# Kernel optimization log

Measured on AMD Instinct MI355X. Metric: run time of the kernel, lower is better.

The kernel has to match this reference:

```python
import jax, jax.numpy as jnp
import numpy as np

N, LQ, D_MODEL, M_HEADS, P_POINTS, H_DIM, W_DIM = 8, 4096, 256, 8, 4, 64, 64


def setup_inputs() -> dict:
    key = jax.random.key(0)
    ks = jax.random.split(key, 9)
    d = D_MODEL
    scale = 1.0 / np.sqrt(d).astype(np.float32)
    return {
        "query": jax.random.normal(ks[0], (N, LQ, d), jnp.float32),
        "reference_points": jax.random.uniform(ks[1], (N, LQ, 2), jnp.float32),
        "input_flatten": jax.random.normal(ks[2], (N, H_DIM * W_DIM, d), jnp.float32),
        "H": H_DIM,
        "W": W_DIM,
        "Wv": jax.random.normal(ks[3], (d, d), jnp.float32) * scale,
        "bv": jnp.zeros((d,), jnp.float32),
        "Woff": jax.random.normal(ks[4], (M_HEADS * P_POINTS * 2, d), jnp.float32) * 0.01,
        "boff": jax.random.normal(ks[5], (M_HEADS * P_POINTS * 2,), jnp.float32) * 0.5,
        "Wa": jax.random.normal(ks[6], (M_HEADS * P_POINTS, d), jnp.float32) * 0.01,
        "ba": jnp.zeros((M_HEADS * P_POINTS,), jnp.float32),
        "Wo": jax.random.normal(ks[7], (d, d), jnp.float32) * scale,
        "bo": jnp.zeros((d,), jnp.float32),
    }


def _bilinear_sample(val, grid, H, W):
    # val: [B, D, H*W]; grid: [B, Lq, P, 2] in [-1, 1] (x, y); align_corners=False, zero padding.
    B, D, _ = val.shape
    _, Lq, P, _ = grid.shape
    x = (grid[..., 0] + 1.0) * (W * 0.5) - 0.5
    y = (grid[..., 1] + 1.0) * (H * 0.5) - 0.5
    x0 = jnp.floor(x)
    y0 = jnp.floor(y)
    x0i = x0.astype(jnp.int32)
    y0i = y0.astype(jnp.int32)
    wx1 = x - x0
    wy1 = y - y0
    out = jnp.zeros((B, D, Lq, P), val.dtype)
    for xi, wx in ((x0i, 1.0 - wx1), (x0i + 1, wx1)):
        for yi, wy in ((y0i, 1.0 - wy1), (y0i + 1, wy1)):
            valid = (xi >= 0) & (xi < W) & (yi >= 0) & (yi < H)
            idx = jnp.clip(yi, 0, H - 1) * W + jnp.clip(xi, 0, W - 1)  # [B, Lq, P]
            g = jnp.take_along_axis(val, idx.reshape(B, 1, Lq * P), axis=2).reshape(B, D, Lq, P)
            w = jnp.where(valid, wx * wy, 0.0)
            out = out + g * w[:, None]
    return out


def reference(query, reference_points, input_flatten, H, W, Wv, bv, Woff, boff, Wa, ba, Wo, bo):
    n, lq, d = query.shape
    m, p = M_HEADS, P_POINTS
    dh = d // m
    value = (input_flatten @ Wv.T + bv).reshape(n, H * W, m, dh)
    offsets = (query @ Woff.T + boff).reshape(n, lq, m, p, 2)
    attw = jax.nn.softmax((query @ Wa.T + ba).reshape(n, lq, m, p), axis=-1)
    normalizer = jnp.array([W, H], dtype=query.dtype)  # [W, H] order per torch code
    loc = reference_points[:, :, None, None, :] + offsets / normalizer
    grid = 2.0 * loc - 1.0  # [n, lq, m, p, 2]
    # value -> [n*m, dh, H*W] matching torch flatten(2).transpose(1,2).reshape
    val = jnp.transpose(value, (0, 2, 3, 1)).reshape(n * m, dh, H * W)
    grd = jnp.transpose(grid, (0, 2, 1, 3, 4)).reshape(n * m, lq, p, 2)
    samp = _bilinear_sample(val, grd, H, W)  # [n*m, dh, lq, p]
    aw = jnp.transpose(attw, (0, 2, 1, 3)).reshape(n * m, 1, lq, p)
    out = (samp * aw).sum(-1).reshape(n, m * dh, lq)
    out = jnp.transpose(out, (0, 2, 1))  # [n, lq, d]
    return out @ Wo.T + bo
```

## Files before the change

kernel.cpp:

```cpp
#include <hip/hip_runtime.h>
#include <math.h>

#define NB   8
#define LQN  4096
#define DM   256
#define MH   8
#define PP   4
#define HH   64
#define WW   64
#define LG   128
#define PW   67
#define PPIX (PW*PW)

typedef __bf16 bf16x8 __attribute__((ext_vector_type(8)));
typedef float  f32x4  __attribute__((ext_vector_type(4)));
typedef unsigned short us8 __attribute__((ext_vector_type(8)));
typedef unsigned short us4 __attribute__((ext_vector_type(4)));

__device__ __forceinline__ unsigned short f2bf(float f) {
    unsigned u = __float_as_uint(f);
    u += 0x7FFFu + ((u >> 16) & 1u);
    return (unsigned short)(u >> 16);
}
__device__ __forceinline__ float bf2f(unsigned short b) {
    return __uint_as_float((unsigned)b << 16);
}

__device__ __forceinline__ void gl2lds16(const void* g, unsigned short* l) {
    __builtin_amdgcn_global_load_lds(
        (const __attribute__((address_space(1))) void*)g,
        (__attribute__((address_space(3))) void*)l,
        16, 0, 0);
}

__device__ __forceinline__ bf16x8 cvt_frag(const unsigned short* s, int row, int kq) {
    const int u0 = row * 8 + ((kq * 2) ^ (row & 7));
    const int u1 = u0 ^ 1;
    const f32x4 a0 = *(const f32x4*)&s[u0 * 8];
    const f32x4 a1 = *(const f32x4*)&s[u1 * 8];
    bf16x8 v;
    v[0] = (__bf16)a0[0]; v[1] = (__bf16)a0[1];
    v[2] = (__bf16)a0[2]; v[3] = (__bf16)a0[3];
    v[4] = (__bf16)a1[0]; v[5] = (__bf16)a1[1];
    v[6] = (__bf16)a1[2]; v[7] = (__bf16)a1[3];
    return v;
}

__global__ __launch_bounds__(256)
void prep_kernel(const float* __restrict__ Wv, const float* __restrict__ Wo,
                 const float* __restrict__ Woff, const float* __restrict__ Wa,
                 const float* __restrict__ boff, const float* __restrict__ ba,
                 unsigned short* __restrict__ Wvh, unsigned short* __restrict__ Woh,
                 unsigned short* __restrict__ Wcath, float* __restrict__ bcat,
                 unsigned short* __restrict__ valueP) {
    const int i = blockIdx.x * 256 + threadIdx.x;
    if (i < 65536) {
        Wvh[i] = f2bf(Wv[i]);
    } else if (i < 131072) {
        const int j = i - 65536;
        Woh[j] = f2bf(Wo[j]);
    } else if (i < 163840) {
        const int j = i - 131072, n = j >> 8, k = j & 255;
        const float v = (n < 64) ? Woff[n * 256 + k]
                                 : ((n < 96) ? Wa[(n - 64) * 256 + k] : 0.f);
        Wcath[j] = f2bf(v);
    } else if (i < 163968) {
        const int n = i - 163840;
        bcat[n] = (n < 64) ? boff[n] : ((n < 96) ? ba[n - 64] : 0.f);
    } else if (i < 163968 + 201216) {
        const int j   = i - 163968;
        const int c4  = j & 63;
        const int pix = j >> 6;
        const int n   = pix / 393;
        const int r   = pix - n * 393;
        int x, y;
        if (r < 201) {
            const int q = r / 67;
            y = (q == 0) ? 0 : (q == 1 ? 65 : 66);
            x = r - q * 67;
        } else {
            const int q = r - 201;
            y = 1 + q / 3;
            const int s = q - (q / 3) * 3;
            x = (s == 0) ? 0 : (s == 1 ? 65 : 66);
        }
        const size_t addr = ((size_t)n * PPIX + (size_t)y * PW + x) * DM + c4 * 4;
        *(ushort4*)&valueP[addr] = make_ushort4(0, 0, 0, 0);
    }
}

__global__ __launch_bounds__(256, 4)
void dual_gemm(const float* __restrict__ Ain, const float* __restrict__ Aq,
               const unsigned short* __restrict__ Wvh,
               const unsigned short* __restrict__ Wcath,
               const float* __restrict__ bv, const float* __restrict__ bcat,
               unsigned short* __restrict__ valueP,
               unsigned short* __restrict__ logitsB) {
    constexpr int K = 256, NK = 8;
    __shared__ unsigned short sA[2][4096];
    __shared__ unsigned short sB[2][4096];

    const int t   = threadIdx.x;
    const int blk = blockIdx.x;
    const bool isVal = (blk < 1024);

    const float* A; const unsigned short* B; const float* bias;
    int brow, bcol;
    if (isVal) {
        const int x   = blk & 7;
        const int idx = blk >> 3;
        brow = x * 4096 + (idx >> 1) * 64;
        bcol = (idx & 1) * 128;
        A = Ain; B = Wvh; bias = bv;
    } else {
        const int blk2 = blk - 1024;
        brow = (blk2 & 7) * 4096 + (blk2 >> 3) * 64;
        bcol = 0;
        A = Aq; B = Wcath; bias = bcat;
    }

    const int srow = t >> 3;
    const int scq  = (t & 7) ^ (srow & 7);
    const float* aG = A + (size_t)(brow + srow) * K + scq * 4;
    const size_t aI = (size_t)32 * K;

    const unsigned short* bG = B + (size_t)(bcol + (t >> 2)) * K + (t & 3) * 8;
    const size_t bI = (size_t)64 * K;

    const int l   = t & 63;
    const int wid = t >> 6;
    const int wr  = wid >> 1, wc = wid & 1;
    const int fr  = l & 15,   kq = l >> 4;

    f32x4 acc[2][4] = {};

#define STAGE(buf, ks_) { const int k0_ = (ks_) * 32;                    \
       gl2lds16(aG + k0_,      &sA[buf][t * 8]);                         \
       gl2lds16(aG + k0_ + aI, &sA[buf][2048 + t * 8]);                  \
       gl2lds16(bG + k0_,      &sB[buf][t * 8]);                         \
       gl2lds16(bG + k0_ + bI, &sB[buf][2048 + t * 8]); }

    STAGE(0, 0);
    STAGE(1, 1);

    for (int ks = 0; ks < NK; ++ks) {
        const int cur = ks & 1;
        if (ks < NK - 1) asm volatile("s_waitcnt vmcnt(4)" ::: "memory");
        else             asm volatile("s_waitcnt vmcnt(0)" ::: "memory");
        __builtin_amdgcn_s_barrier();
        __builtin_amdgcn_sched_barrier(0);

        bf16x8 af[2], bf_[4];
#pragma unroll
        for (int m = 0; m < 2; ++m)
            af[m]  = cvt_frag(sA[cur], wr * 32 + m * 16 + fr, kq);
#pragma unroll
        for (int n = 0; n < 4; ++n)
            bf_[n] = *(const bf16x8*)&sB[cur][(wc * 64 + n * 16 + fr) * 32 + kq * 8];

#pragma unroll
        for (int m = 0; m < 2; ++m)
#pragma unroll
            for (int n = 0; n < 4; ++n)
                acc[m][n] = __builtin_amdgcn_mfma_f32_16x16x32_bf16(
                    bf_[n], af[m], acc[m][n], 0, 0, 0);

        __builtin_amdgcn_sched_barrier(0);
        __builtin_amdgcn_s_barrier();
        if (ks + 2 < NK) STAGE(cur, ks + 2);
    }
#undef STAGE

#pragma unroll
    for (int m = 0; m < 2; ++m) {
        const int row = brow + wr * 32 + m * 16 + fr;
        size_t rbase;
        if (isVal) {
            const int nb_ = row >> 12;
            const int pix = row & 4095;
            const int y   = pix >> 6, x = pix & 63;
            rbase = ((size_t)nb_ * PPIX + (size_t)(y + 1) * PW + (x + 1)) * DM;
        } else {
            rbase = (size_t)row * LG;
        }
#pragma unroll
        for (int n = 0; n < 4; ++n) {
            const int colq = bcol + wc * 64 + n * 16 + kq * 4;
            const float4 b4 = *(const float4*)&bias[colq];
            us4 o;
            o[0] = f2bf(acc[m][n][0] + b4.x);
            o[1] = f2bf(acc[m][n][1] + b4.y);
            o[2] = f2bf(acc[m][n][2] + b4.z);
            o[3] = f2bf(acc[m][n][3] + b4.w);
            *(us4*)&(isVal ? valueP : logitsB)[rbase + colq] = o;
        }
    }
}

__global__ __launch_bounds__(512, 4)
void fused_sample_out(const float* __restrict__ refp,
                      const unsigned short* __restrict__ valueP,
                      const unsigned short* __restrict__ logitsB,
                      const unsigned short* __restrict__ Woh,
                      const float* __restrict__ bo, float* __restrict__ C) {
    constexpr int K = 256, NK = 8;
    extern __shared__ unsigned short smem[];
    unsigned short* sS = smem;
    unsigned short* sB = smem + 16384;

    const int t    = threadIdx.x;
    const int blk  = blockIdx.x;
    const int nb   = blk & 7;
    const int brow = nb * 4096 + (blk >> 3) * 64;
    const int w    = t >> 6;
    const int lane = t & 63;

    {
        const int tp  = lane & 31;
        const int pm  = tp >> 2, ppt = tp & 3;
        const int half = lane >> 5;
        const int c8   = lane & 31;
        const int mh   = c8 >> 2;
        const unsigned short* vbase = valueP + (size_t)nb * (PPIX * DM) + c8 * 8;

        for (int i = 0; i < 8; ++i) {
            const int q = w * 8 + i;
            const int b = brow + q;
            const unsigned short* lg = logitsB + (size_t)b * LG;

            const float rx = refp[(size_t)b * 2 + 0];
            const float ry = refp[(size_t)b * 2 + 1];
            const float ox = bf2f(lg[pm * 8 + ppt * 2 + 0]);
            const float oy = bf2f(lg[pm * 8 + ppt * 2 + 1]);
            const float la = bf2f(lg[64 + tp]);

            const float x = fminf(fmaxf(fmaf(rx, (float)WW, ox) - 0.5f, -1.0f), 64.0f);
            const float y = fminf(fmaxf(fmaf(ry, (float)HH, oy) - 0.5f, -1.0f), 64.0f);

            float mx = fmaxf(la, __shfl_xor(la, 1));
            mx = fmaxf(mx, __shfl_xor(mx, 2));
            const float e = __expf(la - mx);
            float den = e + __shfl_xor(e, 1);
            den += __shfl_xor(den, 2);
            const float wgt = e / den;

            float accv[8] = {};
#pragma unroll
            for (int p = 0; p < PP; ++p) {
                const int   sl = mh * PP + p;
                const float xp = __shfl(x, sl);
                const float yp = __shfl(y, sl);
                const float wp = __shfl(wgt, sl);

                const float x0f = floorf(xp), y0f = floorf(yp);
                const int   x0 = (int)x0f,   y0 = (int)y0f;
                const float wx1 = xp - x0f,  wy1 = yp - y0f;
                const float wy  = half ? wy1 : (1.f - wy1);
                const float wA  = wp * wy * (1.f - wx1);
                const float wB  = wp * wy * wx1;

                const unsigned short* p0 =
                    vbase + (size_t)((y0 + 1 + half) * PW + (x0 + 1)) * DM;
                const us8 gA = *(const us8*)(p0);
                const us8 gB = *(const us8*)(p0 + DM);
#pragma unroll
                for (int j = 0; j < 8; ++j) {
                    accv[j] = fmaf(wA, bf2f(gA[j]), accv[j]);
                    accv[j] = fmaf(wB, bf2f(gB[j]), accv[j]);
                }
            }
#pragma unroll
            for (int j = 0; j < 8; ++j)
                accv[j] += __shfl_xor(accv[j], 32);

            if (half == 0) {
                us8 o;
#pragma unroll
                for (int j = 0; j < 8; ++j) o[j] = f2bf(accv[j]);
                *(us8*)&sS[q * 256 + ((c8 ^ (q & 7)) * 8)] = o;
            }
        }
    }
    __syncthreads();

    const unsigned short* bG = Woh + (size_t)(t >> 2) * K + (t & 3) * 8;
    const size_t rHalf = (size_t)128 * K;

    const int wr = w >> 2, wc = w & 3;
    const int fr = lane & 15, kq = lane >> 4;

    f32x4 acc[2][4] = {};

#define STAGEF(buf, ks_) { const int k0_ = (ks_) * 32;                   \
       gl2lds16(bG + k0_,         &sB[(buf) * 8192 + t * 8]);            \
       gl2lds16(bG + k0_ + rHalf, &sB[(buf) * 8192 + 4096 + t * 8]); }

    STAGEF(0, 0);
    STAGEF(1, 1);

    for (int ks = 0; ks < NK; ++ks) {
        const int cur = ks & 1;
        if (ks < NK - 1) asm volatile("s_waitcnt vmcnt(2)" ::: "memory");
        else             asm volatile("s_waitcnt vmcnt(0)" ::: "memory");
        __builtin_amdgcn_s_barrier();
        __builtin_amdgcn_sched_barrier(0);

        bf16x8 af[2], bfr[4];
#pragma unroll
        for (int m = 0; m < 2; ++m) {
            const int row = wr * 32 + m * 16 + fr;
            const int u   = (ks * 4 + kq) ^ (row & 7);
            af[m] = *(const bf16x8*)&sS[row * 256 + u * 8];
        }
#pragma unroll
        for (int n = 0; n < 4; ++n)
            bfr[n] = *(const bf16x8*)&sB[cur * 8192 + (wc * 64 + n * 16 + fr) * 32 + kq * 8];

#pragma unroll
        for (int m = 0; m < 2; ++m)
#pragma unroll
            for (int n = 0; n < 4; ++n)
                acc[m][n] = __builtin_amdgcn_mfma_f32_16x16x32_bf16(
                    bfr[n], af[m], acc[m][n], 0, 0, 0);

        __builtin_amdgcn_sched_barrier(0);
        __builtin_amdgcn_s_barrier();
        if (ks + 2 < NK) STAGEF(cur, ks + 2);
    }
#undef STAGEF

#pragma unroll
    for (int m = 0; m < 2; ++m) {
        const int row = brow + wr * 32 + m * 16 + fr;
#pragma unroll
        for (int n = 0; n < 4; ++n) {
            const int colq = wc * 64 + n * 16 + kq * 4;
            const float4 bs = *(const float4*)&bo[colq];
            float4 o;
            o.x = acc[m][n][0] + bs.x; o.y = acc[m][n][1] + bs.y;
            o.z = acc[m][n][2] + bs.z; o.w = acc[m][n][3] + bs.w;
            *(float4*)&C[(size_t)row * DM + colq] = o;
        }
    }
}

extern "C" void kernel_launch(void* const* d_in, const int* in_sizes, int n_in,
                              void* d_out, int out_size, void* d_ws, size_t ws_size,
                              hipStream_t stream) {
    const float* query  = (const float*)d_in[0];
    const float* refp   = (const float*)d_in[1];
    const float* inputf = (const float*)d_in[2];
    const float* Wv   = (const float*)d_in[5];
    const float* bv   = (const float*)d_in[6];
    const float* Woff = (const float*)d_in[7];
    const float* boff = (const float*)d_in[8];
    const float* Wa   = (const float*)d_in[9];
    const float* ba   = (const float*)d_in[10];
    const float* Wo   = (const float*)d_in[11];
    const float* bo   = (const float*)d_in[12];
    float* out = (float*)d_out;

    const int Mrows = NB * LQN;

    unsigned short* valueP   = (unsigned short*)d_ws;
    unsigned short* logitsB  = valueP   + (size_t)NB * PPIX * DM;
    unsigned short* Wvh      = logitsB  + (size_t)Mrows * LG;
    unsigned short* Woh      = Wvh      + 65536;
    unsigned short* Wcath    = Woh      + 65536;
    float*          bcat     = (float*)(Wcath + 32768);

    prep_kernel<<<1427, 256, 0, stream>>>(Wv, Wo, Woff, Wa, boff, ba,
                                          Wvh, Woh, Wcath, bcat, valueP);

    dual_gemm<<<1536, 256, 0, stream>>>(inputf, query, Wvh, Wcath, bv, bcat,
                                        valueP, logitsB);

    fused_sample_out<<<512, 512, 65536, stream>>>(refp, valueP, logitsB,
                                                  Woh, bo, out);
}
```

Measured before the change: 59.87 us.

## Fuse offset/attention-logit GEMM into the sampling-output kernel via LDS

Moves the query projection that produces sampling offsets and attention logits out of the combined GEMM launch and into the sampling/output kernel. Each block now computes its own 64x128 logits tile with MFMA and keeps it in LDS rather than writing it to a global buffer and reading it back. The aim is to remove that global round trip and let the value GEMM run alone with fewer blocks. In exchange, dynamic LDS grows to 80 KB per block, which may reduce occupancy. The query GEMM is also no longer overlapped with the value GEMM.

```diff
diff --git a/kernel.cpp b/kernel.cpp
--- a/kernel.cpp
+++ b/kernel.cpp
@@ -8,7 +8,6 @@
 #define PP   4
 #define HH   64
 #define WW   64
-#define LG   128
 #define PW   67
 #define PPIX (PW*PW)
 
@@ -90,41 +89,27 @@
 }
 
 __global__ __launch_bounds__(256, 4)
-void dual_gemm(const float* __restrict__ Ain, const float* __restrict__ Aq,
-               const unsigned short* __restrict__ Wvh,
-               const unsigned short* __restrict__ Wcath,
-               const float* __restrict__ bv, const float* __restrict__ bcat,
-               unsigned short* __restrict__ valueP,
-               unsigned short* __restrict__ logitsB) {
+void value_gemm(const float* __restrict__ Ain,
+                const unsigned short* __restrict__ Wvh,
+                const float* __restrict__ bv,
+                unsigned short* __restrict__ valueP) {
     constexpr int K = 256, NK = 8;
     __shared__ unsigned short sA[2][4096];
     __shared__ unsigned short sB[2][4096];
 
     const int t   = threadIdx.x;
     const int blk = blockIdx.x;
-    const bool isVal = (blk < 1024);
-
-    const float* A; const unsigned short* B; const float* bias;
-    int brow, bcol;
-    if (isVal) {
-        const int x   = blk & 7;
-        const int idx = blk >> 3;
-        brow = x * 4096 + (idx >> 1) * 64;
-        bcol = (idx & 1) * 128;
-        A = Ain; B = Wvh; bias = bv;
-    } else {
-        const int blk2 = blk - 1024;
-        brow = (blk2 & 7) * 4096 + (blk2 >> 3) * 64;
-        bcol = 0;
-        A = Aq; B = Wcath; bias = bcat;
-    }
+    const int xb  = blk & 7;
+    const int idx = blk >> 3;
+    const int brow = xb * 4096 + (idx >> 1) * 64;
+    const int bcol = (idx & 1) * 128;
 
     const int srow = t >> 3;
     const int scq  = (t & 7) ^ (srow & 7);
-    const float* aG = A + (size_t)(brow + srow) * K + scq * 4;
+    const float* aG = Ain + (size_t)(brow + srow) * K + scq * 4;
     const size_t aI = (size_t)32 * K;
 
-    const unsigned short* bG = B + (size_t)(bcol + (t >> 2)) * K + (t & 3) * 8;
+    const unsigned short* bG = Wvh + (size_t)(bcol + (t >> 2)) * K + (t & 3) * 8;
     const size_t bI = (size_t)64 * K;
 
     const int l   = t & 63;
@@ -174,39 +159,37 @@
 #pragma unroll
     for (int m = 0; m < 2; ++m) {
         const int row = brow + wr * 32 + m * 16 + fr;
-        size_t rbase;
-        if (isVal) {
-            const int nb_ = row >> 12;
-            const int pix = row & 4095;
-            const int y   = pix >> 6, x = pix & 63;
-            rbase = ((size_t)nb_ * PPIX + (size_t)(y + 1) * PW + (x + 1)) * DM;
-        } else {
-            rbase = (size_t)row * LG;
-        }
+        const int nb_ = row >> 12;
+        const int pix = row & 4095;
+        const int y   = pix >> 6, x = pix & 63;
+        const size_t rbase =
+            ((size_t)nb_ * PPIX + (size_t)(y + 1) * PW + (x + 1)) * DM;
 #pragma unroll
         for (int n = 0; n < 4; ++n) {
             const int colq = bcol + wc * 64 + n * 16 + kq * 4;
-            const float4 b4 = *(const float4*)&bias[colq];
+            const float4 b4 = *(const float4*)&bv[colq];
             us4 o;
             o[0] = f2bf(acc[m][n][0] + b4.x);
             o[1] = f2bf(acc[m][n][1] + b4.y);
             o[2] = f2bf(acc[m][n][2] + b4.z);
             o[3] = f2bf(acc[m][n][3] + b4.w);
-            *(us4*)&(isVal ? valueP : logitsB)[rbase + colq] = o;
+            *(us4*)&valueP[rbase + colq] = o;
         }
     }
 }
 
 __global__ __launch_bounds__(512, 4)
-void fused_sample_out(const float* __restrict__ refp,
-                      const unsigned short* __restrict__ valueP,
-                      const unsigned short* __restrict__ logitsB,
-                      const unsigned short* __restrict__ Woh,
-                      const float* __restrict__ bo, float* __restrict__ C) {
+void fused_lso(const float* __restrict__ query, const float* __restrict__ refp,
+               const unsigned short* __restrict__ valueP,
+               const unsigned short* __restrict__ Wcath,
+               const float* __restrict__ bcat,
+               const unsigned short* __restrict__ Woh,
+               const float* __restrict__ bo, float* __restrict__ C) {
     constexpr int K = 256, NK = 8;
     extern __shared__ unsigned short smem[];
     unsigned short* sS = smem;
     unsigned short* sB = smem + 16384;
+    unsigned short* sL = smem + 32768;
 
     const int t    = threadIdx.x;
     const int blk  = blockIdx.x;
@@ -214,6 +197,75 @@
     const int brow = nb * 4096 + (blk >> 3) * 64;
     const int w    = t >> 6;
     const int lane = t & 63;
+    const int fr   = lane & 15, kq = lane >> 4;
+
+    {
+        unsigned short* sQ = sS;
+        unsigned short* sW = sS + 8192;
+
+        const int srow = t >> 3;
+        const int scq  = (t & 7) ^ (srow & 7);
+        const float* aG = query + (size_t)(brow + srow) * K + scq * 4;
+        const unsigned short* wG = Wcath + (size_t)(t >> 2) * K + (t & 3) * 8;
+
+        const int wr0 = w >> 2;
+        const int wc0 = w & 3;
+
+        f32x4 acc[2][2] = {};
+
+#define STG0(buf, ks_) { const int k0_ = (ks_) * 32;                     \
+       gl2lds16(aG + k0_, &sQ[(buf) * 4096 + t * 8]);                    \
+       gl2lds16(wG + k0_, &sW[(buf) * 4096 + t * 8]); }
+
+        STG0(0, 0);
+        STG0(1, 1);
+
+        for (int ks = 0; ks < NK; ++ks) {
+            const int cur = ks & 1;
+            if (ks < NK - 1) asm volatile("s_waitcnt vmcnt(2)" ::: "memory");
+            else             asm volatile("s_waitcnt vmcnt(0)" ::: "memory");
+            __builtin_amdgcn_s_barrier();
+            __builtin_amdgcn_sched_barrier(0);
+
+            bf16x8 af[2], bw[2];
+#pragma unroll
+            for (int m = 0; m < 2; ++m)
+                af[m] = cvt_frag(&sQ[cur * 4096], wr0 * 32 + m * 16 + fr, kq);
+#pragma unroll
+            for (int n = 0; n < 2; ++n)
+                bw[n] = *(const bf16x8*)&sW[cur * 4096 +
+                        (wc0 * 32 + n * 16 + fr) * 32 + kq * 8];
+
+#pragma unroll
+            for (int m = 0; m < 2; ++m)
+#pragma unroll
+                for (int n = 0; n < 2; ++n)
+                    acc[m][n] = __builtin_amdgcn_mfma_f32_16x16x32_bf16(
+                        bw[n], af[m], acc[m][n], 0, 0, 0);
+
+            __builtin_amdgcn_sched_barrier(0);
+            __builtin_amdgcn_s_barrier();
+            if (ks + 2 < NK) STG0(cur, ks + 2);
+        }
+#undef STG0
+
+#pragma unroll
+        for (int m = 0; m < 2; ++m) {
+            const int row = wr0 * 32 + m * 16 + fr;
+#pragma unroll
+            for (int n = 0; n < 2; ++n) {
+                const int colq = wc0 * 32 + n * 16 + kq * 4;
+                const float4 b4 = *(const float4*)&bcat[colq];
+                us4 o;
+                o[0] = f2bf(acc[m][n][0] + b4.x);
+                o[1] = f2bf(acc[m][n][1] + b4.y);
+                o[2] = f2bf(acc[m][n][2] + b4.z);
+                o[3] = f2bf(acc[m][n][3] + b4.w);
+                *(us4*)&sL[row * 128 + colq] = o;
+            }
+        }
+    }
+    __syncthreads();
 
     {
         const int tp  = lane & 31;
@@ -226,7 +278,7 @@
         for (int i = 0; i < 8; ++i) {
             const int q = w * 8 + i;
             const int b = brow + q;
-            const unsigned short* lg = logitsB + (size_t)b * LG;
+            const unsigned short* lg = sL + q * 128;
 
             const float rx = refp[(size_t)b * 2 + 0];
             const float ry = refp[(size_t)b * 2 + 1];
@@ -287,7 +339,6 @@
     const size_t rHalf = (size_t)128 * K;
 
     const int wr = w >> 2, wc = w & 3;
-    const int fr = lane & 15, kq = lane >> 4;
 
     f32x4 acc[2][4] = {};
 
@@ -360,21 +411,17 @@
     const float* bo   = (const float*)d_in[12];
     float* out = (float*)d_out;
 
-    const int Mrows = NB * LQN;
-
-    unsigned short* valueP   = (unsigned short*)d_ws;
-    unsigned short* logitsB  = valueP   + (size_t)NB * PPIX * DM;
-    unsigned short* Wvh      = logitsB  + (size_t)Mrows * LG;
-    unsigned short* Woh      = Wvh      + 65536;
-    unsigned short* Wcath    = Woh      + 65536;
-    float*          bcat     = (float*)(Wcath + 32768);
+    unsigned short* valueP = (unsigned short*)d_ws;
+    unsigned short* Wvh    = valueP + (size_t)NB * PPIX * DM;
+    unsigned short* Woh    = Wvh    + 65536;
+    unsigned short* Wcath  = Woh    + 65536;
+    float*          bcat   = (float*)(Wcath + 32768);
 
     prep_kernel<<<1427, 256, 0, stream>>>(Wv, Wo, Woff, Wa, boff, ba,
                                           Wvh, Woh, Wcath, bcat, valueP);
 
-    dual_gemm<<<1536, 256, 0, stream>>>(inputf, query, Wvh, Wcath, bv, bcat,
-                                        valueP, logitsB);
-
-    fused_sample_out<<<512, 512, 65536, stream>>>(refp, valueP, logitsB,
-                                                  Woh, bo, out);
-}
+    value_gemm<<<1024, 256, 0, stream>>>(inputf, Wvh, bv, valueP);
+
+    fused_lso<<<512, 512, 81920, stream>>>(query, refp, valueP, Wcath, bcat,
+                                           Woh, bo, out);
+}
```

Measured after the change: 59.14 us. No clear change (-1.2%).
